# Optimization experiments

Hardware: AMD Instinct MI355X
Metric: run time of the kernel (lower is better)

## Reference

```python
import jax, jax.numpy as jnp
import numpy as np

HIDDEN_DIM = 1024
N_EXPERTS = 4
EPS = 1e-6


def rmsnorm(x, w):
    return x * jax.lax.rsqrt(jnp.mean(x * x, axis=-1, keepdims=True) + EPS) * w


def setup_inputs() -> dict:
    key = jax.random.key(0)
    k1, k2, k3 = jax.random.split(key, 3)
    B, S = 16, 4096
    x = jax.random.normal(k1, (B, S, HIDDEN_DIM), dtype=jnp.float32)
    experts = jax.random.randint(k2, (B,), 0, N_EXPERTS)
    norm1_w = jnp.ones((HIDDEN_DIM,), dtype=jnp.float32)
    norm2_w = jnp.ones((HIDDEN_DIM,), dtype=jnp.float32)
    time_decay_logit = jnp.full((HIDDEN_DIM,), 2.0, dtype=jnp.float32)
    # stacked expert weights [n_experts, out, in] (torch Linear stores [out, in])
    W_experts = jax.random.normal(k3, (N_EXPERTS, HIDDEN_DIM, HIDDEN_DIM), dtype=jnp.float32) * 0.02
    return {"x": x, "experts": experts, "norm1_w": norm1_w,
            "time_decay_logit": time_decay_logit, "norm2_w": norm2_w,
            "W_experts": W_experts}


def reference(x, experts, norm1_w, time_decay_logit, norm2_w, W_experts):
    B, S, D = x.shape
    x_norm = rmsnorm(x, norm1_w)                      # [B,S,D]
    decay = jax.nn.sigmoid(time_decay_logit)          # [D]

    def step(state, x_t):
        state = state * decay + x_t * (1.0 - decay)
        return state, state

    init = jnp.zeros((B, D), dtype=x.dtype)
    _, states = jax.lax.scan(step, init, jnp.swapaxes(x_norm, 0, 1))  # [S,B,D]
    x = x + jnp.swapaxes(states, 0, 1)                # residual add

    pool_state = rmsnorm(x, norm2_w)[:, -1, :]        # [B,D]
    # gather each sample's expert weight and apply: y = relu(x @ W^T)
    W_b = W_experts[experts]                          # [B,out,in]
    out = jax.nn.relu(jnp.einsum('bd,bod->bo', pool_state, W_b))
    return out
```

## Files before the change

### kernel.cpp

```cpp
#include <hip/hip_runtime.h>
#include <math.h>

#define EPS 1e-6f
#define CH_L 16

__device__ __forceinline__ float4 sigmoid4(float4 lg) {
    return make_float4(1.f / (1.f + expf(-lg.x)), 1.f / (1.f + expf(-lg.y)),
                       1.f / (1.f + expf(-lg.z)), 1.f / (1.f + expf(-lg.w)));
}

__device__ __forceinline__ int window_K(float4 dec, int S, int tid, float* red) {
    int wv = tid >> 6, ln = tid & 63;
    float m = fmaxf(fmaxf(dec.x, dec.y), fmaxf(dec.z, dec.w));
    for (int off = 32; off; off >>= 1) m = fmaxf(m, __shfl_xor(m, off));
    if (ln == 0) red[wv] = m;
    __syncthreads();
    float maxd = fmaxf(fmaxf(red[0], red[1]), fmaxf(red[2], red[3]));
    float Kf;
    if (maxd <= 0.f) Kf = 1.f;
    else {
        float lgm = logf(maxd);
        Kf = (lgm >= 0.f) ? (float)S : (logf(1e-12f) / lgm);
    }
    return (Kf >= (float)S) ? S : ((int)Kf + 1);
}

__global__ void k_ema(const float4* __restrict__ x4, const float4* __restrict__ logit4,
                      const float4* __restrict__ w14, float4* __restrict__ partial4,
                      int B, int S, int nchunk) {
    __shared__ float4 sdec[256], scw[256];
    __shared__ float red[4];
    __shared__ float4 sm[4][256];
    int tid = threadIdx.x, wv = tid >> 6, ln = tid & 63;

    float4 dec_t = sigmoid4(logit4[tid]);
    float4 w1 = w14[tid];
    sdec[tid] = dec_t;
    scw[tid] = make_float4((1.f - dec_t.x) * w1.x, (1.f - dec_t.y) * w1.y,
                           (1.f - dec_t.z) * w1.z, (1.f - dec_t.w) * w1.w);
    int K = window_K(dec_t, S, tid, red);

    float4 d4p[4], cwp[4];
#pragma unroll
    for (int k = 0; k < 4; k++) {
        float4 d = sdec[k * 64 + ln];
        float4 cw = scw[k * 64 + ln];
        float4 d2 = make_float4(d.x * d.x, d.y * d.y, d.z * d.z, d.w * d.w);
        d4p[k] = make_float4(d2.x * d2.x, d2.y * d2.y, d2.z * d2.z, d2.w * d2.w);
        float4 pw;
        if (wv == 3)      pw = make_float4(1.f, 1.f, 1.f, 1.f);
        else if (wv == 2) pw = d;
        else if (wv == 1) pw = d2;
        else              pw = make_float4(d2.x * d.x, d2.y * d.y, d2.z * d.z, d2.w * d.w);
        cwp[k] = make_float4(cw.x * pw.x, cw.y * pw.y, cw.z * pw.z, cw.w * pw.w);
    }

    int nact = K / CH_L + 1; if (nact > nchunk) nact = nchunk;
    int total = B * nact;
    for (int i = blockIdx.x; i < total; i += gridDim.x) {
        int b = i / nact, c = i % nact;
        float4 acc[4];
#pragma unroll
        for (int k = 0; k < 4; k++) acc[k] = make_float4(0.f, 0.f, 0.f, 0.f);
        int t0 = S - (c + 1) * CH_L;
#pragma unroll
        for (int j = 0; j < 4; j++) {
            int t = t0 + 4 * j + wv;
            const float4* xp = x4 + ((size_t)b * S + t) * 256;
            float4 xv[4];
#pragma unroll
            for (int k = 0; k < 4; k++) xv[k] = xp[k * 64 + ln];
            float s = 0.f;
#pragma unroll
            for (int k = 0; k < 4; k++)
                s += xv[k].x * xv[k].x + xv[k].y * xv[k].y + xv[k].z * xv[k].z + xv[k].w * xv[k].w;
            for (int m = 1; m < 64; m <<= 1) s += __shfl_xor(s, m);
            float ir = rsqrtf(s * (1.f / 1024.f) + EPS);
#pragma unroll
            for (int k = 0; k < 4; k++) {
                acc[k].x = acc[k].x * d4p[k].x + xv[k].x * (cwp[k].x * ir);
                acc[k].y = acc[k].y * d4p[k].y + xv[k].y * (cwp[k].y * ir);
                acc[k].z = acc[k].z * d4p[k].z + xv[k].z * (cwp[k].z * ir);
                acc[k].w = acc[k].w * d4p[k].w + xv[k].w * (cwp[k].w * ir);
            }
        }
        __syncthreads();
#pragma unroll
        for (int k = 0; k < 4; k++) sm[wv][k * 64 + ln] = acc[k];
        __syncthreads();
        float4 r0 = sm[0][tid], r1 = sm[1][tid], r2 = sm[2][tid], r3 = sm[3][tid];
        partial4[((size_t)b * nchunk + c) * 256 + tid] =
            make_float4(r0.x + r1.x + r2.x + r3.x, r0.y + r1.y + r2.y + r3.y,
                        r0.z + r1.z + r2.z + r3.z, r0.w + r1.w + r2.w + r3.w);
    }
}

__global__ void k_pool(const float4* __restrict__ x4, const float4* __restrict__ logit4,
                       const float4* __restrict__ w24, const float4* __restrict__ partial4,
                       float4* __restrict__ pool4, int S, int nchunk) {
    __shared__ float red[4];
    __shared__ float tot;
    int b = blockIdx.x;
    int tid = threadIdx.x, wv = tid >> 6, ln = tid & 63;
    float4 d = sigmoid4(logit4[tid]);
    int K = window_K(d, S, tid, red);
    int cmax = K / CH_L; if (cmax > nchunk - 1) cmax = nchunk - 1;
    float4 d2 = make_float4(d.x * d.x, d.y * d.y, d.z * d.z, d.w * d.w);
    float4 d4 = make_float4(d2.x * d2.x, d2.y * d2.y, d2.z * d2.z, d2.w * d2.w);
    float4 d8 = make_float4(d4.x * d4.x, d4.y * d4.y, d4.z * d4.z, d4.w * d4.w);
    float4 dL = make_float4(d8.x * d8.x, d8.y * d8.y, d8.z * d8.z, d8.w * d8.w);
    float4 st = make_float4(0.f, 0.f, 0.f, 0.f);
    float4 wgt = make_float4(1.f, 1.f, 1.f, 1.f);
    for (int c = 0; c <= cmax; c++) {
        float4 p = partial4[((size_t)b * nchunk + c) * 256 + tid];
        st.x += p.x * wgt.x; st.y += p.y * wgt.y;
        st.z += p.z * wgt.z; st.w += p.w * wgt.w;
        wgt.x *= dL.x; wgt.y *= dL.y; wgt.z *= dL.z; wgt.w *= dL.w;
    }
    float4 xl = x4[((size_t)b * S + (S - 1)) * 256 + tid];
    float4 y = make_float4(xl.x + st.x, xl.y + st.y, xl.z + st.z, xl.w + st.w);
    float ss = y.x * y.x + y.y * y.y + y.z * y.z + y.w * y.w;
    for (int m = 1; m < 64; m <<= 1) ss += __shfl_xor(ss, m);
    __syncthreads();
    if (ln == 0) red[wv] = ss;
    __syncthreads();
    if (tid == 0) tot = red[0] + red[1] + red[2] + red[3];
    __syncthreads();
    float ir = rsqrtf(tot * (1.f / 1024.f) + EPS);
    float4 w2 = w24[tid];
    pool4[(size_t)b * 256 + tid] = make_float4(y.x * ir * w2.x, y.y * ir * w2.y,
                                               y.z * ir * w2.z, y.w * ir * w2.w);
}

__global__ void k_matmul(const float* __restrict__ pool, const float* __restrict__ W,
                         const int* __restrict__ experts, float* __restrict__ out,
                         int B, int D, int O) {
    __shared__ float4 sp[16][256];
    __shared__ int blist[16];
    __shared__ int snb;
    int e = blockIdx.y;
    int o0 = blockIdx.x * 64;
    int tid = threadIdx.x, wv = tid >> 6, ln = tid & 63;
    if (tid == 0) {
        int nb = 0;
        for (int b = 0; b < B; b++) if (experts[b] == e) blist[nb++] = b;
        snb = nb;
    }
    __syncthreads();
    int nb = snb;
    if (nb == 0) return;
    const float4* pool4 = (const float4*)pool;
    for (int j = 0; j < nb; j++) sp[j][tid] = pool4[(size_t)blist[j] * 256 + tid];
    __syncthreads();
    const float4* Wb = (const float4*)W + (size_t)e * O * 256;
#pragma unroll 4
    for (int rr = 0; rr < 16; rr++) {
        int row = o0 + wv * 16 + rr;
        float4 w4[4];
#pragma unroll
        for (int k = 0; k < 4; k++) w4[k] = Wb[(size_t)row * 256 + k * 64 + ln];
        for (int j = 0; j < nb; j++) {
            float s = 0.f;
#pragma unroll
            for (int k = 0; k < 4; k++) {
                float4 p = sp[j][k * 64 + ln];
                s += w4[k].x * p.x + w4[k].y * p.y + w4[k].z * p.z + w4[k].w * p.w;
            }
            for (int off = 32; off; off >>= 1) s += __shfl_down(s, off);
            if (ln == 0) out[(size_t)blist[j] * O + row] = fmaxf(s, 0.f);
        }
    }
}

extern "C" void kernel_launch(void* const* d_in, const int* in_sizes, int n_in,
                              void* d_out, int out_size, void* d_ws, size_t ws_size,
                              hipStream_t stream) {
    const float* x       = (const float*)d_in[0];
    const int*   experts = (const int*)  d_in[1];
    const float* w1      = (const float*)d_in[2];
    const float* logit   = (const float*)d_in[3];
    const float* w2      = (const float*)d_in[4];
    const float* W       = (const float*)d_in[5];
    float* out = (float*)d_out;

    int B  = in_sizes[1];
    int D  = in_sizes[2];
    int S  = in_sizes[0] / (B * D);
    int O  = D;
    int NE = in_sizes[5] / (D * D);
    int nchunk = S / CH_L;

    float* ws      = (float*)d_ws;
    float* partial = ws;
    float* pool    = partial + (size_t)B * nchunk * D;

    k_ema<<<512, 256, 0, stream>>>((const float4*)x, (const float4*)logit,
                                   (const float4*)w1, (float4*)partial, B, S, nchunk);
    k_pool<<<B, 256, 0, stream>>>((const float4*)x, (const float4*)logit,
                                  (const float4*)w2, (const float4*)partial,
                                  (float4*)pool, S, nchunk);
    k_matmul<<<dim3(O / 64, NE), 256, 0, stream>>>(pool, W, experts, out, B, D, O);
}
```

Baseline: 354.4 us.

## Precompute decay terms once, fuse pooling into expert matmul, widen matmul grid

A single-block prep kernel now computes the sigmoid decay, the scaled input weights, the 16-step decay power and the active chunk count once, and writes them to workspace. The EMA kernel moves from a grid-stride loop to a 2D grid over chunks and batch, where blocks past the active window exit early. The final RMSNorm pooling is folded into the expert matmul kernel, and that kernel uses 16 output rows per block instead of 64, giving four times as many blocks to stream the expert weights. The cost is that each matmul block recomputes the pooled state for its batch rows, and there is one extra small kernel launch.

```diff
diff --git a/kernel.cpp b/kernel.cpp
--- a/kernel.cpp
+++ b/kernel.cpp
@@ -4,47 +4,57 @@
 #define EPS 1e-6f
 #define CH_L 16
 
-__device__ __forceinline__ float4 sigmoid4(float4 lg) {
-    return make_float4(1.f / (1.f + expf(-lg.x)), 1.f / (1.f + expf(-lg.y)),
-                       1.f / (1.f + expf(-lg.z)), 1.f / (1.f + expf(-lg.w)));
-}
-
-__device__ __forceinline__ int window_K(float4 dec, int S, int tid, float* red) {
-    int wv = tid >> 6, ln = tid & 63;
-    float m = fmaxf(fmaxf(dec.x, dec.y), fmaxf(dec.z, dec.w));
+__global__ void k_prep(const float4* __restrict__ logit4, const float4* __restrict__ w14,
+                       float4* __restrict__ decay4, float4* __restrict__ cw4,
+                       float4* __restrict__ dL4, int* __restrict__ nactp,
+                       int S, int nchunk) {
+    int tid = threadIdx.x, wv = tid >> 6, ln = tid & 63;
+    float4 lg = logit4[tid];
+    float4 w1 = w14[tid];
+    float4 d;
+    d.x = 1.f / (1.f + expf(-lg.x));
+    d.y = 1.f / (1.f + expf(-lg.y));
+    d.z = 1.f / (1.f + expf(-lg.z));
+    d.w = 1.f / (1.f + expf(-lg.w));
+    decay4[tid] = d;
+    cw4[tid] = make_float4((1.f - d.x) * w1.x, (1.f - d.y) * w1.y,
+                           (1.f - d.z) * w1.z, (1.f - d.w) * w1.w);
+    float4 d2 = make_float4(d.x * d.x, d.y * d.y, d.z * d.z, d.w * d.w);
+    float4 d4 = make_float4(d2.x * d2.x, d2.y * d2.y, d2.z * d2.z, d2.w * d2.w);
+    float4 d8 = make_float4(d4.x * d4.x, d4.y * d4.y, d4.z * d4.z, d4.w * d4.w);
+    dL4[tid] = make_float4(d8.x * d8.x, d8.y * d8.y, d8.z * d8.z, d8.w * d8.w);
+    float m = fmaxf(fmaxf(d.x, d.y), fmaxf(d.z, d.w));
     for (int off = 32; off; off >>= 1) m = fmaxf(m, __shfl_xor(m, off));
+    __shared__ float red[4];
     if (ln == 0) red[wv] = m;
     __syncthreads();
-    float maxd = fmaxf(fmaxf(red[0], red[1]), fmaxf(red[2], red[3]));
-    float Kf;
-    if (maxd <= 0.f) Kf = 1.f;
-    else {
-        float lgm = logf(maxd);
-        Kf = (lgm >= 0.f) ? (float)S : (logf(1e-12f) / lgm);
-    }
-    return (Kf >= (float)S) ? S : ((int)Kf + 1);
-}
-
-__global__ void k_ema(const float4* __restrict__ x4, const float4* __restrict__ logit4,
-                      const float4* __restrict__ w14, float4* __restrict__ partial4,
-                      int B, int S, int nchunk) {
-    __shared__ float4 sdec[256], scw[256];
-    __shared__ float red[4];
-    __shared__ float4 sm[4][256];
+    if (tid == 0) {
+        float maxd = fmaxf(fmaxf(red[0], red[1]), fmaxf(red[2], red[3]));
+        float Kf;
+        if (maxd <= 0.f) Kf = 1.f;
+        else {
+            float lgm = logf(maxd);
+            Kf = (lgm >= 0.f) ? (float)S : (logf(1e-12f) / lgm);
+        }
+        int K = (Kf >= (float)S) ? S : ((int)Kf + 1);
+        int na = K / CH_L + 1;
+        if (na > nchunk) na = nchunk;
+        *nactp = na;
+    }
+}
+
+__global__ void k_ema(const float4* __restrict__ x4, const float4* __restrict__ decay4,
+                      const float4* __restrict__ cw4, const int* __restrict__ nactp,
+                      float4* __restrict__ partial4, int S, int nchunk) {
+    int c = blockIdx.x, b = blockIdx.y;
+    if (c >= *nactp) return;
     int tid = threadIdx.x, wv = tid >> 6, ln = tid & 63;
 
-    float4 dec_t = sigmoid4(logit4[tid]);
-    float4 w1 = w14[tid];
-    sdec[tid] = dec_t;
-    scw[tid] = make_float4((1.f - dec_t.x) * w1.x, (1.f - dec_t.y) * w1.y,
-                           (1.f - dec_t.z) * w1.z, (1.f - dec_t.w) * w1.w);
-    int K = window_K(dec_t, S, tid, red);
-
     float4 d4p[4], cwp[4];
 #pragma unroll
     for (int k = 0; k < 4; k++) {
-        float4 d = sdec[k * 64 + ln];
-        float4 cw = scw[k * 64 + ln];
+        float4 d = decay4[k * 64 + ln];
+        float4 cw = cw4[k * 64 + ln];
         float4 d2 = make_float4(d.x * d.x, d.y * d.y, d.z * d.z, d.w * d.w);
         d4p[k] = make_float4(d2.x * d2.x, d2.y * d2.y, d2.z * d2.z, d2.w * d2.w);
         float4 pw;
@@ -55,91 +65,54 @@
         cwp[k] = make_float4(cw.x * pw.x, cw.y * pw.y, cw.z * pw.z, cw.w * pw.w);
     }
 
-    int nact = K / CH_L + 1; if (nact > nchunk) nact = nchunk;
-    int total = B * nact;
-    for (int i = blockIdx.x; i < total; i += gridDim.x) {
-        int b = i / nact, c = i % nact;
-        float4 acc[4];
-#pragma unroll
-        for (int k = 0; k < 4; k++) acc[k] = make_float4(0.f, 0.f, 0.f, 0.f);
-        int t0 = S - (c + 1) * CH_L;
-#pragma unroll
-        for (int j = 0; j < 4; j++) {
-            int t = t0 + 4 * j + wv;
-            const float4* xp = x4 + ((size_t)b * S + t) * 256;
-            float4 xv[4];
-#pragma unroll
-            for (int k = 0; k < 4; k++) xv[k] = xp[k * 64 + ln];
-            float s = 0.f;
-#pragma unroll
-            for (int k = 0; k < 4; k++)
-                s += xv[k].x * xv[k].x + xv[k].y * xv[k].y + xv[k].z * xv[k].z + xv[k].w * xv[k].w;
-            for (int m = 1; m < 64; m <<= 1) s += __shfl_xor(s, m);
-            float ir = rsqrtf(s * (1.f / 1024.f) + EPS);
-#pragma unroll
-            for (int k = 0; k < 4; k++) {
-                acc[k].x = acc[k].x * d4p[k].x + xv[k].x * (cwp[k].x * ir);
-                acc[k].y = acc[k].y * d4p[k].y + xv[k].y * (cwp[k].y * ir);
-                acc[k].z = acc[k].z * d4p[k].z + xv[k].z * (cwp[k].z * ir);
-                acc[k].w = acc[k].w * d4p[k].w + xv[k].w * (cwp[k].w * ir);
-            }
-        }
-        __syncthreads();
-#pragma unroll
-        for (int k = 0; k < 4; k++) sm[wv][k * 64 + ln] = acc[k];
-        __syncthreads();
-        float4 r0 = sm[0][tid], r1 = sm[1][tid], r2 = sm[2][tid], r3 = sm[3][tid];
-        partial4[((size_t)b * nchunk + c) * 256 + tid] =
-            make_float4(r0.x + r1.x + r2.x + r3.x, r0.y + r1.y + r2.y + r3.y,
-                        r0.z + r1.z + r2.z + r3.z, r0.w + r1.w + r2.w + r3.w);
-    }
-}
-
-__global__ void k_pool(const float4* __restrict__ x4, const float4* __restrict__ logit4,
-                       const float4* __restrict__ w24, const float4* __restrict__ partial4,
-                       float4* __restrict__ pool4, int S, int nchunk) {
-    __shared__ float red[4];
-    __shared__ float tot;
-    int b = blockIdx.x;
-    int tid = threadIdx.x, wv = tid >> 6, ln = tid & 63;
-    float4 d = sigmoid4(logit4[tid]);
-    int K = window_K(d, S, tid, red);
-    int cmax = K / CH_L; if (cmax > nchunk - 1) cmax = nchunk - 1;
-    float4 d2 = make_float4(d.x * d.x, d.y * d.y, d.z * d.z, d.w * d.w);
-    float4 d4 = make_float4(d2.x * d2.x, d2.y * d2.y, d2.z * d2.z, d2.w * d2.w);
-    float4 d8 = make_float4(d4.x * d4.x, d4.y * d4.y, d4.z * d4.z, d4.w * d4.w);
-    float4 dL = make_float4(d8.x * d8.x, d8.y * d8.y, d8.z * d8.z, d8.w * d8.w);
-    float4 st = make_float4(0.f, 0.f, 0.f, 0.f);
-    float4 wgt = make_float4(1.f, 1.f, 1.f, 1.f);
-    for (int c = 0; c <= cmax; c++) {
-        float4 p = partial4[((size_t)b * nchunk + c) * 256 + tid];
-        st.x += p.x * wgt.x; st.y += p.y * wgt.y;
-        st.z += p.z * wgt.z; st.w += p.w * wgt.w;
-        wgt.x *= dL.x; wgt.y *= dL.y; wgt.z *= dL.z; wgt.w *= dL.w;
-    }
-    float4 xl = x4[((size_t)b * S + (S - 1)) * 256 + tid];
-    float4 y = make_float4(xl.x + st.x, xl.y + st.y, xl.z + st.z, xl.w + st.w);
-    float ss = y.x * y.x + y.y * y.y + y.z * y.z + y.w * y.w;
-    for (int m = 1; m < 64; m <<= 1) ss += __shfl_xor(ss, m);
+    float4 acc[4];
+#pragma unroll
+    for (int k = 0; k < 4; k++) acc[k] = make_float4(0.f, 0.f, 0.f, 0.f);
+    int t0 = S - (c + 1) * CH_L;
+#pragma unroll
+    for (int j = 0; j < 4; j++) {
+        int t = t0 + 4 * j + wv;
+        const float4* xp = x4 + ((size_t)b * S + t) * 256;
+        float4 xv[4];
+#pragma unroll
+        for (int k = 0; k < 4; k++) xv[k] = xp[k * 64 + ln];
+        float s = 0.f;
+#pragma unroll
+        for (int k = 0; k < 4; k++)
+            s += xv[k].x * xv[k].x + xv[k].y * xv[k].y + xv[k].z * xv[k].z + xv[k].w * xv[k].w;
+        for (int m = 1; m < 64; m <<= 1) s += __shfl_xor(s, m);
+        float ir = rsqrtf(s * (1.f / 1024.f) + EPS);
+#pragma unroll
+        for (int k = 0; k < 4; k++) {
+            acc[k].x = acc[k].x * d4p[k].x + xv[k].x * (cwp[k].x * ir);
+            acc[k].y = acc[k].y * d4p[k].y + xv[k].y * (cwp[k].y * ir);
+            acc[k].z = acc[k].z * d4p[k].z + xv[k].z * (cwp[k].z * ir);
+            acc[k].w = acc[k].w * d4p[k].w + xv[k].w * (cwp[k].w * ir);
+        }
+    }
+
+    __shared__ float4 sm[4][256];
+#pragma unroll
+    for (int k = 0; k < 4; k++) sm[wv][k * 64 + ln] = acc[k];
     __syncthreads();
-    if (ln == 0) red[wv] = ss;
-    __syncthreads();
-    if (tid == 0) tot = red[0] + red[1] + red[2] + red[3];
-    __syncthreads();
-    float ir = rsqrtf(tot * (1.f / 1024.f) + EPS);
-    float4 w2 = w24[tid];
-    pool4[(size_t)b * 256 + tid] = make_float4(y.x * ir * w2.x, y.y * ir * w2.y,
-                                               y.z * ir * w2.z, y.w * ir * w2.w);
-}
-
-__global__ void k_matmul(const float* __restrict__ pool, const float* __restrict__ W,
+    float4 r0 = sm[0][tid], r1 = sm[1][tid], r2 = sm[2][tid], r3 = sm[3][tid];
+    partial4[((size_t)b * nchunk + c) * 256 + tid] =
+        make_float4(r0.x + r1.x + r2.x + r3.x, r0.y + r1.y + r2.y + r3.y,
+                    r0.z + r1.z + r2.z + r3.z, r0.w + r1.w + r2.w + r3.w);
+}
+
+__global__ void k_poolmm(const float4* __restrict__ x4, const float4* __restrict__ partial4,
+                         const float4* __restrict__ decay16_4, const float4* __restrict__ w24,
+                         const int* __restrict__ nactp, const float* __restrict__ W,
                          const int* __restrict__ experts, float* __restrict__ out,
-                         int B, int D, int O) {
+                         int B, int S, int nchunk, int O) {
     __shared__ float4 sp[16][256];
     __shared__ int blist[16];
     __shared__ int snb;
+    __shared__ float red[4];
+    __shared__ float tot;
     int e = blockIdx.y;
-    int o0 = blockIdx.x * 64;
+    int o0 = blockIdx.x * 16;
     int tid = threadIdx.x, wv = tid >> 6, ln = tid & 63;
     if (tid == 0) {
         int nb = 0;
@@ -149,13 +122,41 @@
     __syncthreads();
     int nb = snb;
     if (nb == 0) return;
-    const float4* pool4 = (const float4*)pool;
-    for (int j = 0; j < nb; j++) sp[j][tid] = pool4[(size_t)blist[j] * 256 + tid];
-    __syncthreads();
+
+    int cmax = *nactp - 1;
+    if (cmax > nchunk - 1) cmax = nchunk - 1;
+    float4 dL = decay16_4[tid];
+    float4 w2 = w24[tid];
+
+    for (int j = 0; j < nb; j++) {
+        int b = blist[j];
+        float4 st = make_float4(0.f, 0.f, 0.f, 0.f);
+        float4 wgt = make_float4(1.f, 1.f, 1.f, 1.f);
+        const float4* pp = partial4 + (size_t)b * nchunk * 256 + tid;
+        for (int c = 0; c <= cmax; c++) {
+            float4 p = pp[(size_t)c * 256];
+            st.x += p.x * wgt.x; st.y += p.y * wgt.y;
+            st.z += p.z * wgt.z; st.w += p.w * wgt.w;
+            wgt.x *= dL.x; wgt.y *= dL.y; wgt.z *= dL.z; wgt.w *= dL.w;
+        }
+        float4 xl = x4[((size_t)b * S + (S - 1)) * 256 + tid];
+        float4 y = make_float4(xl.x + st.x, xl.y + st.y, xl.z + st.z, xl.w + st.w);
+        float ss = y.x * y.x + y.y * y.y + y.z * y.z + y.w * y.w;
+        for (int m = 1; m < 64; m <<= 1) ss += __shfl_xor(ss, m);
+        if (ln == 0) red[wv] = ss;
+        __syncthreads();
+        if (tid == 0) tot = red[0] + red[1] + red[2] + red[3];
+        __syncthreads();
+        float ir = rsqrtf(tot * (1.f / 1024.f) + EPS);
+        sp[j][tid] = make_float4(y.x * ir * w2.x, y.y * ir * w2.y,
+                                 y.z * ir * w2.z, y.w * ir * w2.w);
+        __syncthreads();
+    }
+
     const float4* Wb = (const float4*)W + (size_t)e * O * 256;
 #pragma unroll 4
-    for (int rr = 0; rr < 16; rr++) {
-        int row = o0 + wv * 16 + rr;
+    for (int rr = 0; rr < 4; rr++) {
+        int row = o0 + wv * 4 + rr;
         float4 w4[4];
 #pragma unroll
         for (int k = 0; k < 4; k++) w4[k] = Wb[(size_t)row * 256 + k * 64 + ln];
@@ -191,13 +192,20 @@
     int nchunk = S / CH_L;
 
     float* ws      = (float*)d_ws;
-    float* partial = ws;
-    float* pool    = partial + (size_t)B * nchunk * D;
-
-    k_ema<<<512, 256, 0, stream>>>((const float4*)x, (const float4*)logit,
-                                   (const float4*)w1, (float4*)partial, B, S, nchunk);
-    k_pool<<<B, 256, 0, stream>>>((const float4*)x, (const float4*)logit,
-                                  (const float4*)w2, (const float4*)partial,
-                                  (float4*)pool, S, nchunk);
-    k_matmul<<<dim3(O / 64, NE), 256, 0, stream>>>(pool, W, experts, out, B, D, O);
-}
+    float* decay   = ws;
+    float* cw      = ws + D;
+    float* dL      = ws + 2 * D;
+    int*   nactp   = (int*)(ws + 3 * D);
+    float* partial = ws + 3 * D + 64;
+
+    k_prep<<<1, 256, 0, stream>>>((const float4*)logit, (const float4*)w1,
+                                  (float4*)decay, (float4*)cw, (float4*)dL,
+                                  nactp, S, nchunk);
+    k_ema<<<dim3(nchunk, B), 256, 0, stream>>>((const float4*)x, (const float4*)decay,
+                                               (const float4*)cw, nactp,
+                                               (float4*)partial, S, nchunk);
+    k_poolmm<<<dim3(O / 16, NE), 256, 0, stream>>>((const float4*)x, (const float4*)partial,
+                                                   (const float4*)dL, (const float4*)w2,
+                                                   nactp, W, experts, out,
+                                                   B, S, nchunk, O);
+}
```

After: 346.3 us. 1.02x faster.
